# Kernel optimization log

Hardware: AMD Instinct MI355X
Metric: run time of the kernel (lower is better)

Reference implementation:

```python
import jax, jax.numpy as jnp
import numpy as np
import math

N_HEAD = 16
HEAD_DIM = 64
LN_EPS = 1e-5
TEMP = 1.0

def _layernorm(x, scale, bias):
    # normalize over last dim (head_dim)
    mu = jnp.mean(x, axis=-1, keepdims=True)
    var = jnp.mean(jnp.square(x - mu), axis=-1, keepdims=True)
    return (x - mu) / jnp.sqrt(var + LN_EPS) * scale + bias

def setup_inputs() -> dict:
    key = jax.random.key(0)
    ks = jax.random.split(key, 3)
    B, S, C = 4, 2048, 1024
    x = jax.random.normal(ks[0], (B, S, C), dtype=jnp.float32)
    w_qkv = jax.random.normal(ks[1], (C, 3 * C), dtype=jnp.float32) * (C ** -0.5)
    w_proj = jax.random.normal(ks[2], (C, C), dtype=jnp.float32) * (C ** -0.5)
    return {
        "x": x,
        "w_qkv": w_qkv,
        "w_proj": w_proj,
        "q_scale": jnp.ones((HEAD_DIM,), jnp.float32),
        "q_bias": jnp.zeros((HEAD_DIM,), jnp.float32),
        "k_scale": jnp.ones((HEAD_DIM,), jnp.float32),
        "k_bias": jnp.zeros((HEAD_DIM,), jnp.float32),
    }

def reference(x, w_qkv, w_proj, q_scale, q_bias, k_scale, k_bias):
    B, S, C = x.shape
    H, D = N_HEAD, HEAD_DIM
    # qkv projection -> [B,S,3,H,D] -> [3,B,H,S,D]
    qkv = (x @ w_qkv).reshape(B, S, 3, H, D).transpose(2, 0, 3, 1, 4)
    q = _layernorm(qkv[0], q_scale, q_bias)
    k = _layernorm(qkv[1], k_scale, k_bias)
    v = qkv[2]
    # temperature-scaled logits, stable softmax
    inv = 1.0 / (math.sqrt(D) * max(TEMP, 1e-6))
    logits = jnp.einsum('bhqd,bhkd->bhqk', q, k) * inv
    att = jax.nn.softmax(logits, axis=-1)
    # entropy stats (track_stats=True path)
    s_raw = -jnp.sum(att * jnp.log(att + 1e-9), axis=-1)  # [B,H,S]
    batch_entropies = jnp.mean(s_raw / math.log(S), axis=(1, 2))  # [B]
    out = jnp.einsum('bhqk,bhkd->bhqd', att, v).transpose(0, 2, 1, 3).reshape(B, S, C)
    return out @ w_proj, batch_entropies
```

## Files before the change

kernel.cpp:

```cpp
#include <hip/hip_runtime.h>
#include <hip/hip_bf16.h>
#include <math.h>

#define CB 4
#define CS 2048
#define CC 1024
#define CH 16
#define CD 64
#define CBS (CB*CS)

typedef unsigned short u16;
typedef __bf16 bf16x8 __attribute__((ext_vector_type(8)));
typedef float f32x4 __attribute__((ext_vector_type(4)));
typedef float f32x16 __attribute__((ext_vector_type(16)));
typedef unsigned short u16x4 __attribute__((ext_vector_type(4)));
typedef unsigned short u16x8 __attribute__((ext_vector_type(8)));
typedef unsigned u32x2 __attribute__((ext_vector_type(2)));

__device__ __forceinline__ u16 f2bf(float f){
  union { float f; unsigned u; } v; v.f = f;
  unsigned r = v.u + 0x7FFFu + ((v.u >> 16) & 1u);
  return (u16)(r >> 16);
}
__device__ __forceinline__ unsigned pack2bf(float a, float b){
  __hip_bfloat162 h = __float22bfloat162_rn(make_float2(a, b));
  union { __hip_bfloat162 h; unsigned u; } c; c.h = h; return c.u;
}
__device__ __forceinline__ f32x4 mfma16(bf16x8 a, bf16x8 b, f32x4 c){
  return __builtin_amdgcn_mfma_f32_16x16x32_bf16(a, b, c, 0, 0, 0);
}
__device__ __forceinline__ f32x16 mfma32(bf16x8 a, bf16x8 b, f32x16 c){
  return __builtin_amdgcn_mfma_f32_32x32x16_bf16(a, b, c, 0, 0, 0);
}
__device__ __forceinline__ void gload16(const u16* g, u16* lds_base_uniform){
  __builtin_amdgcn_global_load_lds(
      (const __attribute__((address_space(1))) unsigned int*)g,
      (__attribute__((address_space(3))) unsigned int*)lds_base_uniform, 16, 0, 0);
}

__global__ __launch_bounds__(256) void convert_x_kernel(
    const float* __restrict__ x, u16* __restrict__ xb, float* __restrict__ zero4){
  if (blockIdx.x == 0 && threadIdx.x < 4) zero4[threadIdx.x] = 0.0f;
  size_t i = ((size_t)blockIdx.x*256 + threadIdx.x)*8;
  float4 a = *(const float4*)(x+i);
  float4 b = *(const float4*)(x+i+4);
  u16x8 o = { f2bf(a.x),f2bf(a.y),f2bf(a.z),f2bf(a.w),
              f2bf(b.x),f2bf(b.y),f2bf(b.z),f2bf(b.w) };
  *(u16x8*)(xb+i) = o;
}

template<int K, int N>
__global__ __launch_bounds__(256) void transpose_convert_kernel(
    const float* __restrict__ w, u16* __restrict__ wt){
  __shared__ u16 tile[64][65];
  const int nb = N/64;
  int tk0 = (blockIdx.x / nb) * 64;
  int tn0 = (blockIdx.x % nb) * 64;
  int t = threadIdx.x;
  for (int i = 0; i < 4; i++) {
    int r = i*16 + (t>>4);
    int c = (t&15)*4;
    float4 v = *(const float4*)(w + (size_t)(tk0+r)*N + tn0 + c);
    tile[c+0][r]=f2bf(v.x); tile[c+1][r]=f2bf(v.y);
    tile[c+2][r]=f2bf(v.z); tile[c+3][r]=f2bf(v.w);
  }
  __syncthreads();
  for (int i = 0; i < 4; i++) {
    int r = i*16 + (t>>4);
    int c = (t&15)*4;
    u16x4 o = { tile[r][c+0], tile[r][c+1], tile[r][c+2], tile[r][c+3] };
    *(u16x4*)(wt + (size_t)(tn0+r)*K + tk0 + c) = o;
  }
}

__global__ __launch_bounds__(256) void transpose_v_kernel(
    const u16* __restrict__ vb, u16* __restrict__ vtb){
  __shared__ u16 tile[64][72];
  int bh = blockIdx.x >> 5;
  int st = blockIdx.x & 31;
  int t = threadIdx.x;
  const u16* src = vb + (size_t)bh*CS*CD + (size_t)st*64*CD;
  int r = t>>2, c = (t&3)*16;
  *(u16x8*)&tile[r][c]   = *(const u16x8*)(src + (size_t)r*CD + c);
  *(u16x8*)&tile[r][c+8] = *(const u16x8*)(src + (size_t)r*CD + c + 8);
  __syncthreads();
  int d = t>>2, s = (t&3)*16;
  u16x8 o0, o1;
  for (int j=0;j<8;j++){ o0[j] = tile[s+j][d]; o1[j] = tile[s+8+j][d]; }
  u16* dst = vtb + (size_t)bh*CD*CS + (size_t)d*CS + st*64 + s;
  *(u16x8*)dst = o0;
  *(u16x8*)(dst+8) = o1;
}

__global__ __launch_bounds__(256, 2) void gemm_qkv_ln_kernel(
    const u16* __restrict__ xb, const u16* __restrict__ wqkvT,
    const float* __restrict__ qsc, const float* __restrict__ qbi,
    const float* __restrict__ ksc, const float* __restrict__ kbi,
    u16* __restrict__ qb, u16* __restrict__ kb, u16* __restrict__ vb){
  __shared__ u16 al[128*64];
  __shared__ u16 bl[128*64];
  int t = threadIdx.x;
  int wv = t >> 6, lane = t & 63, lo = lane & 15, q4 = lane >> 4;
  int m0 = blockIdx.x * 128;
  int n0 = blockIdx.y * 128;
  int srow = lane >> 3, scol = (lane & 7) * 8;
  const u16* ag = xb    + (size_t)(m0 + srow)*CC + scol;
  const u16* bg = wqkvT + (size_t)(n0 + srow)*CC + scol;

  f32x4 acc[2][8];
  for (int i=0;i<2;i++) for (int j=0;j<8;j++) acc[i][j] = (f32x4){0.f,0.f,0.f,0.f};

  for (int kk = 0; kk < 16; kk++){
    int k0 = kk * 64;
    for (int i = 0; i < 4; i++){
      int inst = i*4 + wv;
      gload16(ag + (size_t)inst*8*CC + k0, al + inst*512);
      gload16(bg + (size_t)inst*8*CC + k0, bl + inst*512);
    }
    __syncthreads();
    for (int ksI = 0; ksI < 2; ksI++){
      int koff = ksI*32 + q4*8;
      bf16x8 a0 = *(const bf16x8*)&al[(wv*32      + lo)*64 + koff];
      bf16x8 a1 = *(const bf16x8*)&al[(wv*32 + 16 + lo)*64 + koff];
      for (int nt=0; nt<8; nt++){
        bf16x8 b = *(const bf16x8*)&bl[(nt*16 + lo)*64 + koff];
        acc[0][nt] = mfma16(a0, b, acc[0][nt]);
        acc[1][nt] = mfma16(a1, b, acc[1][nt]);
      }
    }
    __syncthreads();
  }

  int three = n0 >> 10;
  int h0 = (n0 & 1023) >> 6;
  const float* scp = (three == 0) ? qsc : ksc;
  const float* bip = (three == 0) ? qbi : kbi;
  float outscale = (three == 0) ? 0.125f * 1.44269504088896f : 1.0f;
  u16* dst = (three == 0) ? qb : (three == 1 ? kb : vb);

  for (int rt = 0; rt < 2; rt++){
    int tg = m0 + wv*32 + rt*16 + q4*4;
    for (int hf = 0; hf < 2; hf++){
      int h = h0 + hf;
      for (int r = 0; r < 4; r++){
        int token = tg + r;
        int bb = token >> 11, ss = token & (CS-1);
        size_t base = (((size_t)(bb*CH + h))*CS + ss)*CD;
        if (three < 2){
          float s1 = 0.f, s2 = 0.f;
          for (int j=0;j<4;j++){ float v = acc[rt][hf*4+j][r]; s1 += v; s2 += v*v; }
          for (int off=8; off>=1; off>>=1){
            s1 += __shfl_xor(s1, off, 16);
            s2 += __shfl_xor(s2, off, 16);
          }
          float mean = s1 * (1.f/64.f);
          float var  = s2 * (1.f/64.f) - mean*mean;
          float rstd = rsqrtf(var + 1e-5f);
          for (int j=0;j<4;j++){
            int d = j*16 + lo;
            float v = (acc[rt][hf*4+j][r] - mean) * rstd * scp[d] + bip[d];
            dst[base + d] = f2bf(v * outscale);
          }
        } else {
          for (int j=0;j<4;j++){
            int d = j*16 + lo;
            dst[base + d] = f2bf(acc[rt][hf*4+j][r]);
          }
        }
      }
    }
  }
}

__global__ __launch_bounds__(256, 4) void attention_kernel(
    const u16* __restrict__ qb, const u16* __restrict__ kb,
    const u16* __restrict__ vtb, u16* __restrict__ attnb, float* __restrict__ ent){
  __shared__ __align__(16) u16 kl[2][64*64];
  __shared__ __align__(16) u16 vl[2][64*64];
  __shared__ __align__(16) float zl[4][32];
  int t = threadIdx.x;
  int wv = t >> 6, lane = t & 63;
  int col = lane & 31, hi = lane >> 5;
  int n = blockIdx.x;
  int xc = n & 7, j = n >> 3;
  int bh = xc + 8*(j >> 4);
  int qt = j & 15;
  int bI = bh >> 4;
  int q0w = qt*128 + wv*32;
  const u16* qbp = qb  + (size_t)bh * CS * CD;
  const u16* kbp = kb  + (size_t)bh * CS * CD;
  const u16* vbp = vtb + (size_t)bh * CD * CS;

  int srow  = lane >> 3;
  int sslot = (lane & 7) ^ srow;

  bf16x8 qf[4];
  for (int ks=0;ks<4;ks++)
    qf[ks] = *(const bf16x8*)(qbp + (size_t)(q0w + col)*CD + ks*16 + hi*8);

  f32x16 o[2];
  for (int nt=0;nt<2;nt++) for (int i=0;i<16;i++) o[nt][i] = 0.f;
  float zacc = 0.f, tacc = 0.f;

  for (int c=0;c<2;c++){
    int chunk = wv*2 + c;
    int row = chunk*8 + srow;
    gload16(kbp + (size_t)row*CD + sslot*8, &kl[0][chunk*512]);
    gload16(vbp + (size_t)row*CS + sslot*8, &vl[0][chunk*512]);
  }

  const int cshift = (col & 7);

  for (int it = 0; it < 32; it++){
    const int cur = it & 1, nxt = cur ^ 1;
    __syncthreads();
    if (it < 31){
      int skn = (it+1)*64;
      for (int c=0;c<2;c++){
        int chunk = wv*2 + c;
        int row = chunk*8 + srow;
        gload16(kbp + (size_t)(skn + row)*CD + sslot*8, &kl[nxt][chunk*512]);
        gload16(vbp + (size_t)row*CS + skn + sslot*8, &vl[nxt][chunk*512]);
      }
    }

    bf16x8 kfr[2][4], vfr[2][4];
    for (int mt=0;mt<2;mt++)
      for (int ks=0;ks<4;ks++)
        kfr[mt][ks] = *(const bf16x8*)&kl[cur][(mt*32+col)*64 + (((2*ks+hi)^cshift)<<3)];
    for (int nt=0;nt<2;nt++)
      for (int ks=0;ks<4;ks++)
        vfr[nt][ks] = *(const bf16x8*)&vl[cur][(nt*32+col)*64 + (((2*ks+hi)^cshift)<<3)];

    f32x16 sf[2];
    for (int mt=0;mt<2;mt++) for (int i=0;i<16;i++) sf[mt][i] = 0.f;
    for (int ks=0;ks<4;ks++){
      sf[0] = mfma32(kfr[0][ks], qf[ks], sf[0]);
      sf[1] = mfma32(kfr[1][ks], qf[ks], sf[1]);
    }

    for (int mt=0;mt<2;mt++){
      for (int ksl=0; ksl<2; ksl++){
        float p[2][4];
        for (int gg=0; gg<2; gg++){
          int g = 2*ksl + gg;
          float l0 = sf[mt][g*4+0], l1 = sf[mt][g*4+1],
                l2 = sf[mt][g*4+2], l3 = sf[mt][g*4+3];
          float p0 = __builtin_amdgcn_exp2f(l0);
          float p1 = __builtin_amdgcn_exp2f(l1);
          float p2 = __builtin_amdgcn_exp2f(l2);
          float p3 = __builtin_amdgcn_exp2f(l3);
          zacc += (p0+p1)+(p2+p3);
          tacc += (p0*l0+p1*l1)+(p2*l2+p3*l3);
          p[gg][0]=p0; p[gg][1]=p1; p[gg][2]=p2; p[gg][3]=p3;
        }
        unsigned x0 = pack2bf(p[0][0], p[0][1]);
        unsigned x1 = pack2bf(p[0][2], p[0][3]);
        unsigned y0 = pack2bf(p[1][0], p[1][1]);
        unsigned y1 = pack2bf(p[1][2], p[1][3]);
        u32x2 s0 = __builtin_amdgcn_permlane32_swap(x0, y0, false, false);
        u32x2 s1 = __builtin_amdgcn_permlane32_swap(x1, y1, false, false);
        union { unsigned u[4]; bf16x8 v; } ap;
        ap.u[0] = s0[0]; ap.u[1] = s1[0]; ap.u[2] = s0[1]; ap.u[3] = s1[1];
        int ks = mt*2 + ksl;
        o[0] = mfma32(ap.v, vfr[0][ks], o[0]);
        o[1] = mfma32(ap.v, vfr[1][ks], o[1]);
      }
    }
  }

  float z2 = zacc + __shfl_xor(zacc, 32);
  float t2 = tacc + __shfl_xor(tacc, 32);
  float invz = 1.f / z2;
  if (hi == 0) zl[wv][col] = invz;

  float srowv = 0.69314718055995f * (__builtin_amdgcn_logf(z2) - t2 * invz);
  float ev = (hi == 0) ? srowv : 0.f;
  for (int off=1; off<=32; off<<=1) ev += __shfl_xor(ev, off);
  if (lane == 0){
    float entscale = 1.0f / ((float)CH * (float)CS * logf((float)CS));
    atomicAdd(&ent[bI], ev * entscale);
  }

  u16* obase = attnb + ((size_t)bh*CS + q0w)*CD;
  for (int nt=0;nt<2;nt++){
    for (int g=0;g<4;g++){
      f32x4 iz = *(const f32x4*)&zl[wv][g*8 + hi*4];
      for (int r=0;r<4;r++){
        int qrow = 8*g + 4*hi + r;
        obase[(size_t)qrow*CD + nt*32 + col] = f2bf(o[nt][g*4+r] * iz[r]);
      }
    }
  }
}

__global__ __launch_bounds__(256, 2) void gemm_out_kernel(
    const u16* __restrict__ attnH, const u16* __restrict__ wprojT,
    float* __restrict__ out){
  __shared__ u16 al[128*64];
  __shared__ u16 bl[128*64];
  int t = threadIdx.x;
  int wv = t >> 6, lane = t & 63, lo = lane & 15, q4 = lane >> 4;
  int m0 = blockIdx.x * 128;
  int n0 = blockIdx.y * 128;
  int b  = m0 >> 11, s0 = m0 & (CS-1);
  int srow = lane >> 3, scol = (lane & 7) * 8;
  const u16* bg = wprojT + (size_t)(n0 + srow)*CC + scol;

  f32x4 acc[2][8];
  for (int i=0;i<2;i++) for (int j=0;j<8;j++) acc[i][j] = (f32x4){0.f,0.f,0.f,0.f};

  for (int kk = 0; kk < 16; kk++){
    const u16* abase = attnH + ((size_t)(b*CH + kk)*CS + s0 + srow)*CD + scol;
    for (int i = 0; i < 4; i++){
      int inst = i*4 + wv;
      gload16(abase + (size_t)inst*8*CD, al + inst*512);
      gload16(bg + (size_t)inst*8*CC + kk*64, bl + inst*512);
    }
    __syncthreads();
    for (int ksI = 0; ksI < 2; ksI++){
      int koff = ksI*32 + q4*8;
      bf16x8 a0 = *(const bf16x8*)&al[(wv*32      + lo)*64 + koff];
      bf16x8 a1 = *(const bf16x8*)&al[(wv*32 + 16 + lo)*64 + koff];
      for (int nt=0; nt<8; nt++){
        bf16x8 b2 = *(const bf16x8*)&bl[(nt*16 + lo)*64 + koff];
        acc[0][nt] = mfma16(a0, b2, acc[0][nt]);
        acc[1][nt] = mfma16(a1, b2, acc[1][nt]);
      }
    }
    __syncthreads();
  }

  for (int rt=0;rt<2;rt++){
    for (int r=0;r<4;r++){
      int row = m0 + wv*32 + rt*16 + q4*4 + r;
      for (int nt=0;nt<8;nt++)
        out[(size_t)row*CC + n0 + nt*16 + lo] = acc[rt][nt][r];
    }
  }
}

extern "C" void kernel_launch(void* const* d_in, const int* in_sizes, int n_in,
                              void* d_out, int out_size, void* d_ws, size_t ws_size,
                              hipStream_t stream) {
  const float* x      = (const float*)d_in[0];
  const float* w_qkv  = (const float*)d_in[1];
  const float* w_proj = (const float*)d_in[2];
  const float* q_scale= (const float*)d_in[3];
  const float* q_bias = (const float*)d_in[4];
  const float* k_scale= (const float*)d_in[5];
  const float* k_bias = (const float*)d_in[6];
  float* out = (float*)d_out;
  float* ent = out + (size_t)CBS * CC;

  u16* xb     = (u16*)d_ws;
  u16* wqkvT  = xb     + (size_t)CBS*CC;
  u16* wprojT = wqkvT  + (size_t)3*CC*CC;
  u16* qb     = wprojT + (size_t)CC*CC;
  u16* kb     = qb + (size_t)CB*CH*CS*CD;
  u16* vb     = kb + (size_t)CB*CH*CS*CD;
  u16* vbT    = xb;
  u16* attn   = vb;

  convert_x_kernel<<<dim3(CBS*CC/(256*8)), 256, 0, stream>>>(x, xb, ent);
  transpose_convert_kernel<CC, 3*CC><<<dim3((CC/64)*(3*CC/64)), 256, 0, stream>>>(w_qkv, wqkvT);
  transpose_convert_kernel<CC, CC><<<dim3((CC/64)*(CC/64)), 256, 0, stream>>>(w_proj, wprojT);
  gemm_qkv_ln_kernel<<<dim3(CBS/128, 3*CC/128), 256, 0, stream>>>(
      xb, wqkvT, q_scale, q_bias, k_scale, k_bias, qb, kb, vb);
  transpose_v_kernel<<<dim3(CB*CH*(CS/64)), 256, 0, stream>>>(vb, vbT);
  attention_kernel<<<dim3(CB*CH*(CS/128)), 256, 0, stream>>>(qb, kb, vbT, attn, ent);
  gemm_out_kernel<<<dim3(CBS/128, CC/128), 256, 0, stream>>>(attn, wprojT, out);
}
```

Measured before the change: 359.0 us.

## Use two-wave attention blocks with 64 query rows per wave

The attention kernel now runs 128 threads per block instead of 256, and each wave handles 64 query rows as two 32-row groups. Each K/V fragment read from LDS is therefore reused across twice as many queries, halving LDS read traffic per FLOP. The LDS swizzle now also XORs in the row group, and s_setprio raises priority around the MFMA sections. In exchange each wave holds more accumulator registers and each block carries fewer waves, which may lower occupancy and latency hiding.

```diff
diff --git a/kernel.cpp b/kernel.cpp
--- a/kernel.cpp
+++ b/kernel.cpp
@@ -172,12 +172,12 @@
   }
 }
 
-__global__ __launch_bounds__(256, 4) void attention_kernel(
+__global__ __launch_bounds__(128, 2) void attention_kernel(
     const u16* __restrict__ qb, const u16* __restrict__ kb,
     const u16* __restrict__ vtb, u16* __restrict__ attnb, float* __restrict__ ent){
   __shared__ __align__(16) u16 kl[2][64*64];
   __shared__ __align__(16) u16 vl[2][64*64];
-  __shared__ __align__(16) float zl[4][32];
+  __shared__ __align__(16) float zl[2][2][32];
   int t = threadIdx.x;
   int wv = t >> 6, lane = t & 63;
   int col = lane & 31, hi = lane >> 5;
@@ -186,73 +186,97 @@
   int bh = xc + 8*(j >> 4);
   int qt = j & 15;
   int bI = bh >> 4;
-  int q0w = qt*128 + wv*32;
+  int q0w = qt*128 + wv*64;
   const u16* qbp = qb  + (size_t)bh * CS * CD;
   const u16* kbp = kb  + (size_t)bh * CS * CD;
   const u16* vbp = vtb + (size_t)bh * CD * CS;
 
-  int srow  = lane >> 3;
-  int sslot = (lane & 7) ^ srow;
-
-  bf16x8 qf[4];
-  for (int ks=0;ks<4;ks++)
-    qf[ks] = *(const bf16x8*)(qbp + (size_t)(q0w + col)*CD + ks*16 + hi*8);
-
-  f32x16 o[2];
-  for (int nt=0;nt<2;nt++) for (int i=0;i<16;i++) o[nt][i] = 0.f;
-  float zacc = 0.f, tacc = 0.f;
-
-  for (int c=0;c<2;c++){
-    int chunk = wv*2 + c;
-    int row = chunk*8 + srow;
-    gload16(kbp + (size_t)row*CD + sslot*8, &kl[0][chunk*512]);
-    gload16(vbp + (size_t)row*CS + sslot*8, &vl[0][chunk*512]);
-  }
-
-  const int cshift = (col & 7);
+  int srow = lane >> 3;
+  int sl   = lane & 7;
+
+  bf16x8 qf[2][4];
+  #pragma unroll
+  for (int qg=0; qg<2; qg++)
+    #pragma unroll
+    for (int ks=0; ks<4; ks++)
+      qf[qg][ks] = *(const bf16x8*)(qbp + (size_t)(q0w + qg*32 + col)*CD + ks*16 + hi*8);
+
+  f32x16 o[2][2];
+  #pragma unroll
+  for (int nt=0;nt<2;nt++)
+    #pragma unroll
+    for (int qg=0;qg<2;qg++)
+      #pragma unroll
+      for (int i=0;i<16;i++) o[nt][qg][i] = 0.f;
+  float zacc[2] = {0.f, 0.f}, tacc[2] = {0.f, 0.f};
+
+  #pragma unroll
+  for (int c=0;c<4;c++){
+    int chunk = wv*4 + c;
+    int slot  = sl ^ srow ^ chunk;
+    int row   = chunk*8 + srow;
+    gload16(kbp + (size_t)row*CD + slot*8, &kl[0][chunk*512]);
+    gload16(vbp + (size_t)row*CS + slot*8, &vl[0][chunk*512]);
+  }
+
+  const int ckey = (col & 7) ^ (col >> 3);
 
   for (int it = 0; it < 32; it++){
     const int cur = it & 1, nxt = cur ^ 1;
     __syncthreads();
     if (it < 31){
       int skn = (it+1)*64;
-      for (int c=0;c<2;c++){
-        int chunk = wv*2 + c;
-        int row = chunk*8 + srow;
-        gload16(kbp + (size_t)(skn + row)*CD + sslot*8, &kl[nxt][chunk*512]);
-        gload16(vbp + (size_t)row*CS + skn + sslot*8, &vl[nxt][chunk*512]);
-      }
-    }
-
-    bf16x8 kfr[2][4], vfr[2][4];
-    for (int mt=0;mt<2;mt++)
-      for (int ks=0;ks<4;ks++)
-        kfr[mt][ks] = *(const bf16x8*)&kl[cur][(mt*32+col)*64 + (((2*ks+hi)^cshift)<<3)];
-    for (int nt=0;nt<2;nt++)
-      for (int ks=0;ks<4;ks++)
-        vfr[nt][ks] = *(const bf16x8*)&vl[cur][(nt*32+col)*64 + (((2*ks+hi)^cshift)<<3)];
-
-    f32x16 sf[2];
-    for (int mt=0;mt<2;mt++) for (int i=0;i<16;i++) sf[mt][i] = 0.f;
-    for (int ks=0;ks<4;ks++){
-      sf[0] = mfma32(kfr[0][ks], qf[ks], sf[0]);
-      sf[1] = mfma32(kfr[1][ks], qf[ks], sf[1]);
-    }
-
-    for (int mt=0;mt<2;mt++){
-      for (int ksl=0; ksl<2; ksl++){
-        float p[2][4];
-        for (int gg=0; gg<2; gg++){
-          int g = 2*ksl + gg;
-          float l0 = sf[mt][g*4+0], l1 = sf[mt][g*4+1],
-                l2 = sf[mt][g*4+2], l3 = sf[mt][g*4+3];
+      #pragma unroll
+      for (int c=0;c<4;c++){
+        int chunk = wv*4 + c;
+        int slot  = sl ^ srow ^ chunk;
+        int row   = chunk*8 + srow;
+        gload16(kbp + (size_t)(skn + row)*CD + slot*8, &kl[nxt][chunk*512]);
+        gload16(vbp + (size_t)row*CS + skn + slot*8, &vl[nxt][chunk*512]);
+      }
+    }
+
+    #pragma unroll
+    for (int mt=0; mt<2; mt++){
+      bf16x8 kfr[4], vfr[2][2];
+      #pragma unroll
+      for (int ks=0; ks<4; ks++)
+        kfr[ks] = *(const bf16x8*)&kl[cur][(mt*32+col)*64 + (((2*ks+hi) ^ ckey ^ (mt<<2))<<3)];
+      #pragma unroll
+      for (int nt=0; nt<2; nt++)
+        #pragma unroll
+        for (int ksl=0; ksl<2; ksl++){
+          int ks = mt*2 + ksl;
+          vfr[nt][ksl] = *(const bf16x8*)&vl[cur][(nt*32+col)*64 + (((2*ks+hi) ^ ckey ^ (nt<<2))<<3)];
+        }
+
+      f32x16 sfq[2];
+      #pragma unroll
+      for (int qg=0;qg<2;qg++)
+        #pragma unroll
+        for (int i=0;i<16;i++) sfq[qg][i] = 0.f;
+      __builtin_amdgcn_s_setprio(1);
+      #pragma unroll
+      for (int ks=0; ks<4; ks++){
+        sfq[0] = mfma32(kfr[ks], qf[0][ks], sfq[0]);
+        sfq[1] = mfma32(kfr[ks], qf[1][ks], sfq[1]);
+      }
+      __builtin_amdgcn_s_setprio(0);
+
+      #pragma unroll
+      for (int qg=0; qg<2; qg++){
+        float p[4][4];
+        #pragma unroll
+        for (int g=0; g<4; g++){
+          float l0 = sfq[qg][g*4+0], l1 = sfq[qg][g*4+1],
+                l2 = sfq[qg][g*4+2], l3 = sfq[qg][g*4+3];
           float p0 = __builtin_amdgcn_exp2f(l0);
           float p1 = __builtin_amdgcn_exp2f(l1);
           float p2 = __builtin_amdgcn_exp2f(l2);
           float p3 = __builtin_amdgcn_exp2f(l3);
-          zacc += (p0+p1)+(p2+p3);
-          tacc += (p0*l0+p1*l1)+(p2*l2+p3*l3);
-          p[gg][0]=p0; p[gg][1]=p1; p[gg][2]=p2; p[gg][3]=p3;
+          zacc[qg] += (p0+p1)+(p2+p3);
+          tacc[qg] += (p0*l0+p1*l1)+(p2*l2+p3*l3);
+          p[g][0]=p0; p[g][1]=p1; p[g][2]=p2; p[g][3]=p3;
         }
         unsigned x0 = pack2bf(p[0][0], p[0][1]);
         unsigned x1 = pack2bf(p[0][2], p[0][3]);
@@ -260,35 +284,57 @@
         unsigned y1 = pack2bf(p[1][2], p[1][3]);
         u32x2 s0 = __builtin_amdgcn_permlane32_swap(x0, y0, false, false);
         u32x2 s1 = __builtin_amdgcn_permlane32_swap(x1, y1, false, false);
-        union { unsigned u[4]; bf16x8 v; } ap;
-        ap.u[0] = s0[0]; ap.u[1] = s1[0]; ap.u[2] = s0[1]; ap.u[3] = s1[1];
-        int ks = mt*2 + ksl;
-        o[0] = mfma32(ap.v, vfr[0][ks], o[0]);
-        o[1] = mfma32(ap.v, vfr[1][ks], o[1]);
-      }
-    }
-  }
-
-  float z2 = zacc + __shfl_xor(zacc, 32);
-  float t2 = tacc + __shfl_xor(tacc, 32);
-  float invz = 1.f / z2;
-  if (hi == 0) zl[wv][col] = invz;
-
-  float srowv = 0.69314718055995f * (__builtin_amdgcn_logf(z2) - t2 * invz);
-  float ev = (hi == 0) ? srowv : 0.f;
+        union { unsigned u[4]; bf16x8 v; } ap0;
+        ap0.u[0] = s0[0]; ap0.u[1] = s1[0]; ap0.u[2] = s0[1]; ap0.u[3] = s1[1];
+        unsigned x2 = pack2bf(p[2][0], p[2][1]);
+        unsigned x3 = pack2bf(p[2][2], p[2][3]);
+        unsigned y2 = pack2bf(p[3][0], p[3][1]);
+        unsigned y3 = pack2bf(p[3][2], p[3][3]);
+        u32x2 s2 = __builtin_amdgcn_permlane32_swap(x2, y2, false, false);
+        u32x2 s3 = __builtin_amdgcn_permlane32_swap(x3, y3, false, false);
+        union { unsigned u[4]; bf16x8 v; } ap1;
+        ap1.u[0] = s2[0]; ap1.u[1] = s3[0]; ap1.u[2] = s2[1]; ap1.u[3] = s3[1];
+        __builtin_amdgcn_s_setprio(1);
+        o[0][qg] = mfma32(ap0.v, vfr[0][0], o[0][qg]);
+        o[1][qg] = mfma32(ap0.v, vfr[1][0], o[1][qg]);
+        o[0][qg] = mfma32(ap1.v, vfr[0][1], o[0][qg]);
+        o[1][qg] = mfma32(ap1.v, vfr[1][1], o[1][qg]);
+        __builtin_amdgcn_s_setprio(0);
+      }
+    }
+  }
+
+  float srw[2];
+  #pragma unroll
+  for (int qg=0; qg<2; qg++){
+    float z2 = zacc[qg] + __shfl_xor(zacc[qg], 32);
+    float t2 = tacc[qg] + __shfl_xor(tacc[qg], 32);
+    float invz = 1.f / z2;
+    if (hi == 0) zl[wv][qg][col] = invz;
+    srw[qg] = 0.69314718055995f * (__builtin_amdgcn_logf(z2) - t2 * invz);
+  }
+  float ev = (hi == 0) ? (srw[0] + srw[1]) : 0.f;
   for (int off=1; off<=32; off<<=1) ev += __shfl_xor(ev, off);
   if (lane == 0){
     float entscale = 1.0f / ((float)CH * (float)CS * logf((float)CS));
     atomicAdd(&ent[bI], ev * entscale);
   }
 
+  __syncthreads();
+
   u16* obase = attnb + ((size_t)bh*CS + q0w)*CD;
-  for (int nt=0;nt<2;nt++){
-    for (int g=0;g<4;g++){
-      f32x4 iz = *(const f32x4*)&zl[wv][g*8 + hi*4];
-      for (int r=0;r<4;r++){
-        int qrow = 8*g + 4*hi + r;
-        obase[(size_t)qrow*CD + nt*32 + col] = f2bf(o[nt][g*4+r] * iz[r]);
+  #pragma unroll
+  for (int qg=0; qg<2; qg++){
+    #pragma unroll
+    for (int nt=0; nt<2; nt++){
+      #pragma unroll
+      for (int g=0; g<4; g++){
+        f32x4 iz = *(const f32x4*)&zl[wv][qg][g*8 + hi*4];
+        #pragma unroll
+        for (int r=0; r<4; r++){
+          int qrow = qg*32 + 8*g + 4*hi + r;
+          obase[(size_t)qrow*CD + nt*32 + col] = f2bf(o[nt][qg][g*4+r] * iz[r]);
+        }
       }
     }
   }
@@ -368,6 +414,6 @@
   gemm_qkv_ln_kernel<<<dim3(CBS/128, 3*CC/128), 256, 0, stream>>>(
       xb, wqkvT, q_scale, q_bias, k_scale, k_bias, qb, kb, vb);
   transpose_v_kernel<<<dim3(CB*CH*(CS/64)), 256, 0, stream>>>(vb, vbT);
-  attention_kernel<<<dim3(CB*CH*(CS/128)), 256, 0, stream>>>(qb, kb, vbT, attn, ent);
+  attention_kernel<<<dim3(CB*CH*(CS/128)), 128, 0, stream>>>(qb, kb, vbT, attn, ent);
   gemm_out_kernel<<<dim3(CBS/128, CC/128), 256, 0, stream>>>(attn, wprojT, out);
 }
```

After: 386.7 us. 1.08x slower.
